# Kernel tuning notes

Measured on AMD Instinct MI355X. Metric: run time of the kernel, lower is better.

## Reference

```python
import jax, jax.numpy as jnp
import numpy as np

DIM = 1024
HEADS = 16
SCALE = DIM ** (-0.5)  # note: full dim, matching original module


def setup_inputs() -> dict:
    key = jax.random.key(0)
    k1, k2, k3, k4 = jax.random.split(key, 4)
    x = jax.random.normal(k1, (8, 1024, DIM), dtype=jnp.float32)
    w_qkv = jax.random.normal(k2, (DIM, 3 * DIM), dtype=jnp.float32) * (DIM ** -0.5)
    w_out = jax.random.normal(k3, (DIM, DIM), dtype=jnp.float32) * (DIM ** -0.5)
    b_out = jax.random.normal(k4, (DIM,), dtype=jnp.float32) * 0.01
    return {"x": x, "w_qkv": w_qkv, "w_out": w_out, "b_out": b_out}


def reference(x, w_qkv, w_out, b_out):
    b, n, dim = x.shape
    h = HEADS
    d = dim // h
    qkv = x @ w_qkv  # [b, n, 3*dim]
    q, k, v = jnp.split(qkv, 3, axis=-1)
    # 'b n (h d) -> b h n d'
    def to_heads(t):
        return t.reshape(b, n, h, d).transpose(0, 2, 1, 3)
    q, k, v = to_heads(q), to_heads(k), to_heads(v)
    dots = jnp.einsum('bhid,bhjd->bhij', q, k) * SCALE
    attn = jax.nn.softmax(dots, axis=-1)
    out = jnp.einsum('bhij,bhjd->bhid', attn, v)
    out = out.transpose(0, 2, 1, 3).reshape(b, n, dim)  # 'b h n d -> b n (h d)'
    return out @ w_out + b_out  # dropout is identity (rate=0 / eval)
```

## Files before the change

kernel.cpp:

```cpp
#include <hip/hip_runtime.h>

typedef __bf16 bf16x8 __attribute__((ext_vector_type(8)));
typedef __bf16 bf16x4 __attribute__((ext_vector_type(4)));
typedef float  f32x4  __attribute__((ext_vector_type(4)));

#define MFMA16(a, b, c) __builtin_amdgcn_mfma_f32_16x16x32_bf16(a, b, c, 0, 0, 0)
#define GLL(gp, lp) __builtin_amdgcn_global_load_lds( \
    (__attribute__((address_space(1))) void*)(gp),    \
    (__attribute__((address_space(3))) void*)(lp), 16, 0, 0)
#define WAITBAR(N) asm volatile("s_waitcnt vmcnt(" #N ") lgkmcnt(0)\n\ts_barrier" ::: "memory")

__global__ __launch_bounds__(256) void cast_x_kernel(const float* __restrict__ in,
                                                     __bf16* __restrict__ out) {
  int i = blockIdx.x * 256 + threadIdx.x;
  const float4 v = ((const float4*)in)[i];
  bf16x4 o = {(__bf16)v.x, (__bf16)v.y, (__bf16)v.z, (__bf16)v.w};
  ((bf16x4*)out)[i] = o;
}

__global__ void transpose_cast_kernel(const float* __restrict__ in,
                                      __bf16* __restrict__ out,
                                      int rows, int cols) {
  __shared__ float tile[32][33];
  int tx = threadIdx.x, ty = threadIdx.y;
  int x = blockIdx.x * 32 + tx;
  int y0 = blockIdx.y * 32;
#pragma unroll
  for (int i = 0; i < 32; i += 8)
    tile[ty + i][tx] = in[(y0 + ty + i) * cols + x];
  __syncthreads();
  int ox = y0 + tx;
  int oy0 = blockIdx.x * 32;
#pragma unroll
  for (int i = 0; i < 32; i += 8)
    out[(oy0 + ty + i) * rows + ox] = (__bf16)tile[tx][ty + i];
}

#define QSCALE 0.045084220027780106f
__global__ __launch_bounds__(256) void gemm_bt_kernel(
    const __bf16* __restrict__ A, const __bf16* __restrict__ Bt, int mode, int nxg,
    __bf16* __restrict__ qo, __bf16* __restrict__ ko, __bf16* __restrict__ vo,
    float* __restrict__ outp, const float* __restrict__ bias) {
  __shared__ __bf16 LDS[3][2][4096];
  const int tid = threadIdx.x;
  const int id = blockIdx.x;
  const int xcd = id & 7, s = id >> 3;
  const int bx = xcd * nxg + (nxg == 3 ? s % 3 : 0);
  const int by = (nxg == 3 ? s / 3 : s);
  const int m0 = by * 128, n0 = bx * 128;
  const int w = tid >> 6, lane = tid & 63;
  const int quad = lane >> 4, l15 = lane & 15;
  const int wm = (w >> 1) * 64, wn = (w & 1) * 64;
  f32x4 acc[4][4] = {};
  const int sr = tid >> 2;
  const int sc = (tid & 3) * 8;
  const __bf16* ag = A + (m0 + sr) * 1024 + sc;
  const __bf16* bg = Bt + (n0 + sr) * 1024 + sc;

  auto stage = [&](int T, int b) {
    const int kk = T * 32;
    GLL(ag + kk,             &LDS[b][0][0] + w * 512);
    GLL(ag + 64 * 1024 + kk, &LDS[b][0][0] + 2048 + w * 512);
    GLL(bg + kk,             &LDS[b][1][0] + w * 512);
    GLL(bg + 64 * 1024 + kk, &LDS[b][1][0] + 2048 + w * 512);
  };
  auto compute = [&](int b) {
    const __bf16* Asb = &LDS[b][0][0];
    const __bf16* Bsb = &LDS[b][1][0];
    bf16x8 af[4], bfr[4];
#pragma unroll
    for (int i = 0; i < 4; ++i)
      af[i] = *(const bf16x8*)(Asb + (wm + i * 16 + l15) * 32 + quad * 8);
#pragma unroll
    for (int j = 0; j < 4; ++j)
      bfr[j] = *(const bf16x8*)(Bsb + (wn + j * 16 + l15) * 32 + quad * 8);
#pragma unroll
    for (int i = 0; i < 4; ++i)
#pragma unroll
      for (int j = 0; j < 4; ++j)
        acc[i][j] = MFMA16(af[i], bfr[j], acc[i][j]);
  };

  stage(0, 0);
  stage(1, 1);
  WAITBAR(4);
  for (int g = 0; g < 10; ++g) {
    const int t = g * 3;
    stage(t + 2, 2); compute(0); WAITBAR(4);
    stage(t + 3, 0); compute(1); WAITBAR(4);
    stage(t + 4, 1); compute(2); WAITBAR(4);
  }
  compute(0);
  asm volatile("s_waitcnt vmcnt(0) lgkmcnt(0)\n\ts_barrier" ::: "memory");
  compute(1);
  __syncthreads();

  const int gcw = n0 + wn;
  float* T = (float*)(&LDS[0][0][0]) + w * 1088;
  if (mode == 0) {
    const int which = gcw >> 10;
    const int h = (gcw & 1023) >> 6;
    if (which == 2) {
#pragma unroll
      for (int i = 0; i < 4; ++i) {
        int gm = m0 + wm + i * 16 + quad * 4;
        int b = gm >> 10, n = gm & 1023;
        __bf16* vb = vo + ((long)(b * 16 + h) * 64) * 1024 + n;
#pragma unroll
        for (int j = 0; j < 4; ++j) {
          int dd = j * 16 + l15;
          bf16x4 pv = {(__bf16)acc[i][j][0], (__bf16)acc[i][j][1],
                       (__bf16)acc[i][j][2], (__bf16)acc[i][j][3]};
          *(bf16x4*)(vb + (long)dd * 1024) = pv;
        }
      }
    } else {
      __bf16* dst = (which == 0) ? qo : ko;
      const float scl = (which == 0) ? QSCALE : 1.0f;
#pragma unroll
      for (int i = 0; i < 4; ++i) {
#pragma unroll
        for (int j = 0; j < 4; ++j)
#pragma unroll
          for (int r = 0; r < 4; ++r)
            T[(quad * 4 + r) * 68 + j * 16 + l15] = acc[i][j][r];
        const float* Tr = T + l15 * 68 + quad * 16;
        f32x4 c0 = *(const f32x4*)(Tr);
        f32x4 c1 = *(const f32x4*)(Tr + 4);
        f32x4 c2 = *(const f32x4*)(Tr + 8);
        f32x4 c3 = *(const f32x4*)(Tr + 12);
        int gm = m0 + wm + i * 16 + l15;
        int b = gm >> 10, n = gm & 1023;
        __bf16* p = dst + ((long)((b * 16 + h) * 1024 + n)) * 64 + quad * 16;
        bf16x8 o0 = {(__bf16)(c0[0] * scl), (__bf16)(c0[1] * scl),
                     (__bf16)(c0[2] * scl), (__bf16)(c0[3] * scl),
                     (__bf16)(c1[0] * scl), (__bf16)(c1[1] * scl),
                     (__bf16)(c1[2] * scl), (__bf16)(c1[3] * scl)};
        bf16x8 o1 = {(__bf16)(c2[0] * scl), (__bf16)(c2[1] * scl),
                     (__bf16)(c2[2] * scl), (__bf16)(c2[3] * scl),
                     (__bf16)(c3[0] * scl), (__bf16)(c3[1] * scl),
                     (__bf16)(c3[2] * scl), (__bf16)(c3[3] * scl)};
        *(bf16x8*)p = o0;
        *(bf16x8*)(p + 8) = o1;
      }
    }
  } else {
    const int cb = gcw;
    f32x4 bv[4];
#pragma unroll
    for (int c = 0; c < 4; ++c)
      bv[c] = *(const f32x4*)(bias + cb + quad * 16 + c * 4);
#pragma unroll
    for (int i = 0; i < 4; ++i) {
#pragma unroll
      for (int j = 0; j < 4; ++j)
#pragma unroll
        for (int r = 0; r < 4; ++r)
          T[(quad * 4 + r) * 68 + j * 16 + l15] = acc[i][j][r];
      const float* Tr = T + l15 * 68 + quad * 16;
      int gm = m0 + wm + i * 16 + l15;
      float* p = outp + (long)gm * 1024 + cb + quad * 16;
#pragma unroll
      for (int c = 0; c < 4; ++c) {
        f32x4 v = *(const f32x4*)(Tr + c * 4);
        v += bv[c];
        *(f32x4*)(p + c * 4) = v;
      }
    }
  }
}

__global__ __launch_bounds__(256, 4) void attn_kernel(
    const __bf16* __restrict__ q, const __bf16* __restrict__ k,
    const __bf16* __restrict__ vt, __bf16* __restrict__ ao) {
  __shared__ __bf16 Ks[128 * 64];
  __shared__ __bf16 Vs[64 * 128];
  __shared__ __bf16 Ps[4][32 * 32];
  const int tid = threadIdx.x;
  const int bh = blockIdx.x & 127, qt = blockIdx.x >> 7;
  const int w = tid >> 6, lane = tid & 63;
  const int quad = lane >> 4, l15 = lane & 15;
  const int qrow = qt * 128 + w * 32;
  const __bf16* qb = q + (bh * 1024 + qrow) * 64;
  bf16x8 qf[2][2];
#pragma unroll
  for (int f = 0; f < 2; ++f) {
    qf[f][0] = *(const bf16x8*)(qb + (f * 16 + l15) * 64 + quad * 8);
    qf[f][1] = *(const bf16x8*)(qb + (f * 16 + l15) * 64 + 32 + quad * 8);
  }
  f32x4 o[2][4] = {};
  float rs0 = 0.f, rs1 = 0.f;
  const int krow = tid >> 3, kg8 = tid & 7;
  const __bf16* kg = k + (bh * 1024 + krow) * 64 + kg8 * 8;
  const int ksw = ((kg8 ^ (krow & 7)) * 8);
  const int vrow = tid >> 2, vg4 = tid & 3;
  const __bf16* vg = vt + (bh * 64 + vrow) * 1024 + vg4 * 8;
  const int kfs0 = (quad ^ (l15 & 7)) * 8;
  const int kfs1 = ((4 + quad) ^ (l15 & 7)) * 8;
  __bf16* pw = Ps[w];
  const int psw = quad ^ (l15 & 3);
  for (int j0 = 0; j0 < 1024; j0 += 128) {
    bf16x8 kv[4], vv[4];
#pragma unroll
    for (int p = 0; p < 4; ++p) kv[p] = *(const bf16x8*)(kg + (j0 + p * 32) * 64);
#pragma unroll
    for (int p = 0; p < 4; ++p) vv[p] = *(const bf16x8*)(vg + j0 + p * 32);
    __syncthreads();
#pragma unroll
    for (int p = 0; p < 4; ++p)
      *(bf16x8*)(Ks + (krow + p * 32) * 64 + ksw) = kv[p];
#pragma unroll
    for (int p = 0; p < 4; ++p)
      *(bf16x8*)(Vs + vrow * 128 + (((p * 4 + vg4) ^ (vrow & 15)) * 8)) = vv[p];
    __syncthreads();
    bf16x4 pk[2][8];
#pragma unroll
    for (int t = 0; t < 8; ++t) {
      const __bf16* kr = Ks + (t * 16 + l15) * 64;
      bf16x8 kf0 = *(const bf16x8*)(kr + kfs0);
      bf16x8 kf1 = *(const bf16x8*)(kr + kfs1);
      f32x4 z0 = {}, z1 = {};
      z0 = MFMA16(kf0, qf[0][0], z0);
      z0 = MFMA16(kf1, qf[0][1], z0);
      z1 = MFMA16(kf0, qf[1][0], z1);
      z1 = MFMA16(kf1, qf[1][1], z1);
      float p00 = exp2f(z0[0]), p01 = exp2f(z0[1]), p02 = exp2f(z0[2]), p03 = exp2f(z0[3]);
      float p10 = exp2f(z1[0]), p11 = exp2f(z1[1]), p12 = exp2f(z1[2]), p13 = exp2f(z1[3]);
      rs0 += (p00 + p01) + (p02 + p03);
      rs1 += (p10 + p11) + (p12 + p13);
      pk[0][t] = (bf16x4){(__bf16)p00, (__bf16)p01, (__bf16)p02, (__bf16)p03};
      pk[1][t] = (bf16x4){(__bf16)p10, (__bf16)p11, (__bf16)p12, (__bf16)p13};
    }
#pragma unroll
    for (int Q = 0; Q < 4; ++Q) {
#pragma unroll
      for (int f = 0; f < 2; ++f)
#pragma unroll
        for (int tl = 0; tl < 2; ++tl) {
          int g = (2 * tl + (quad >> 1)) ^ (l15 & 3);
          *(bf16x4*)(pw + (f * 16 + l15) * 32 + g * 8 + (quad & 1) * 4) = pk[f][2 * Q + tl];
        }
      bf16x8 pf0 = *(const bf16x8*)(pw + l15 * 32 + psw * 8);
      bf16x8 pf1 = *(const bf16x8*)(pw + (16 + l15) * 32 + psw * 8);
#pragma unroll
      for (int dt = 0; dt < 4; ++dt) {
        bf16x8 vf = *(const bf16x8*)(Vs + (dt * 16 + l15) * 128 + (((Q * 4 + quad) ^ l15) * 8));
        o[0][dt] = MFMA16(pf0, vf, o[0][dt]);
        o[1][dt] = MFMA16(pf1, vf, o[1][dt]);
      }
    }
  }
  rs0 += __shfl_xor(rs0, 16); rs0 += __shfl_xor(rs0, 32);
  rs1 += __shfl_xor(rs1, 16); rs1 += __shfl_xor(rs1, 32);
  const int b = bh >> 4, h = bh & 15;
  const int qbase = quad << 4;
#pragma unroll
  for (int r = 0; r < 4; ++r) {
    int src = qbase | (quad * 4 + r);
    float inv0 = 1.0f / __shfl(rs0, src);
    float inv1 = 1.0f / __shfl(rs1, src);
    long row0 = b * 1024 + qrow + quad * 4 + r;
    long row1 = row0 + 16;
#pragma unroll
    for (int dt = 0; dt < 4; ++dt) {
      ao[row0 * 1024 + h * 64 + dt * 16 + l15] = (__bf16)(o[0][dt][r] * inv0);
      ao[row1 * 1024 + h * 64 + dt * 16 + l15] = (__bf16)(o[1][dt][r] * inv1);
    }
  }
}

extern "C" void kernel_launch(void* const* d_in, const int* in_sizes, int n_in,
                              void* d_out, int out_size, void* d_ws, size_t ws_size,
                              hipStream_t stream) {
  const float* x = (const float*)d_in[0];
  const float* w_qkv = (const float*)d_in[1];
  const float* w_out = (const float*)d_in[2];
  const float* b_out = (const float*)d_in[3];
  float* out = (float*)d_out;

  char* ws = (char*)d_ws;
  __bf16* xb    = (__bf16*)(ws);
  __bf16* wqkvt = (__bf16*)(ws + 16777216);
  __bf16* woutt = (__bf16*)(ws + 23068672);
  __bf16* qw    = (__bf16*)(ws + 25165824);
  __bf16* kw    = (__bf16*)(ws + 41943040);
  __bf16* vw    = (__bf16*)(ws + 58720256);
  __bf16* ao    = xb;

  cast_x_kernel<<<8192, 256, 0, stream>>>(x, xb);
  transpose_cast_kernel<<<dim3(96, 32), dim3(32, 8), 0, stream>>>(w_qkv, wqkvt, 1024, 3072);
  transpose_cast_kernel<<<dim3(32, 32), dim3(32, 8), 0, stream>>>(w_out, woutt, 1024, 1024);
  gemm_bt_kernel<<<1536, 256, 0, stream>>>(xb, wqkvt, 0, 3, qw, kw, vw, nullptr, nullptr);
  attn_kernel<<<1024, 256, 0, stream>>>(qw, kw, vw, ao);
  gemm_bt_kernel<<<512, 256, 0, stream>>>(ao, woutt, 1, 1, nullptr, nullptr, nullptr, out, b_out);
}
```

Before: 277.3 us.

## Prefetch next K/V tile, interleave QK and PV, vectorize attention output stores

The attention kernel now issues global loads for the next K/V tile right after the LDS barrier, so they overlap with the current tile's compute instead of stalling at the top of each iteration. QK^T/exp generation is interleaved per Q-chunk with the PV MFMAs, with s_setprio raised around MFMA groups and the hardware exp2 builtin used. The output epilogue stages the accumulators through LDS to emit 16-byte bf16 stores instead of scattered 2-byte stores. This costs extra registers held across the loop and an added barrier plus LDS round trip at the end.

Measured after the change: 242.9 us. -12.4%, faster.

```diff
diff --git a/kernel.cpp b/kernel.cpp
--- a/kernel.cpp
+++ b/kernel.cpp
@@ -173,9 +173,10 @@
 __global__ __launch_bounds__(256, 4) void attn_kernel(
     const __bf16* __restrict__ q, const __bf16* __restrict__ k,
     const __bf16* __restrict__ vt, __bf16* __restrict__ ao) {
-  __shared__ __bf16 Ks[128 * 64];
-  __shared__ __bf16 Vs[64 * 128];
+  __shared__ __bf16 KV[2][128 * 64];
   __shared__ __bf16 Ps[4][32 * 32];
+  __bf16* const Ks = KV[0];
+  __bf16* const Vs = KV[1];
   const int tid = threadIdx.x;
   const int bh = blockIdx.x & 127, qt = blockIdx.x >> 7;
   const int w = tid >> 6, lane = tid & 63;
@@ -192,79 +193,102 @@
   float rs0 = 0.f, rs1 = 0.f;
   const int krow = tid >> 3, kg8 = tid & 7;
   const __bf16* kg = k + (bh * 1024 + krow) * 64 + kg8 * 8;
-  const int ksw = ((kg8 ^ (krow & 7)) * 8);
+  const int ksw = (kg8 ^ (krow & 7)) * 8;
   const int vrow = tid >> 2, vg4 = tid & 3;
   const __bf16* vg = vt + (bh * 64 + vrow) * 1024 + vg4 * 8;
   const int kfs0 = (quad ^ (l15 & 7)) * 8;
   const int kfs1 = ((4 + quad) ^ (l15 & 7)) * 8;
-  __bf16* pw = Ps[w];
+  __bf16* const pw = Ps[w];
   const int psw = quad ^ (l15 & 3);
-  for (int j0 = 0; j0 < 1024; j0 += 128) {
-    bf16x8 kv[4], vv[4];
-#pragma unroll
-    for (int p = 0; p < 4; ++p) kv[p] = *(const bf16x8*)(kg + (j0 + p * 32) * 64);
-#pragma unroll
-    for (int p = 0; p < 4; ++p) vv[p] = *(const bf16x8*)(vg + j0 + p * 32);
+
+  bf16x8 kvr[4], vvr[4];
+#pragma unroll
+  for (int p = 0; p < 4; ++p) kvr[p] = *(const bf16x8*)(kg + (p * 32) * 64);
+#pragma unroll
+  for (int p = 0; p < 4; ++p) vvr[p] = *(const bf16x8*)(vg + p * 32);
+
+  for (int jt = 0; jt < 8; ++jt) {
     __syncthreads();
 #pragma unroll
     for (int p = 0; p < 4; ++p)
-      *(bf16x8*)(Ks + (krow + p * 32) * 64 + ksw) = kv[p];
+      *(bf16x8*)(Ks + (krow + p * 32) * 64 + ksw) = kvr[p];
 #pragma unroll
     for (int p = 0; p < 4; ++p)
-      *(bf16x8*)(Vs + vrow * 128 + (((p * 4 + vg4) ^ (vrow & 15)) * 8)) = vv[p];
+      *(bf16x8*)(Vs + vrow * 128 + (((p * 4 + vg4) ^ (vrow & 15)) * 8)) = vvr[p];
     __syncthreads();
-    bf16x4 pk[2][8];
-#pragma unroll
-    for (int t = 0; t < 8; ++t) {
-      const __bf16* kr = Ks + (t * 16 + l15) * 64;
-      bf16x8 kf0 = *(const bf16x8*)(kr + kfs0);
-      bf16x8 kf1 = *(const bf16x8*)(kr + kfs1);
-      f32x4 z0 = {}, z1 = {};
-      z0 = MFMA16(kf0, qf[0][0], z0);
-      z0 = MFMA16(kf1, qf[0][1], z0);
-      z1 = MFMA16(kf0, qf[1][0], z1);
-      z1 = MFMA16(kf1, qf[1][1], z1);
-      float p00 = exp2f(z0[0]), p01 = exp2f(z0[1]), p02 = exp2f(z0[2]), p03 = exp2f(z0[3]);
-      float p10 = exp2f(z1[0]), p11 = exp2f(z1[1]), p12 = exp2f(z1[2]), p13 = exp2f(z1[3]);
-      rs0 += (p00 + p01) + (p02 + p03);
-      rs1 += (p10 + p11) + (p12 + p13);
-      pk[0][t] = (bf16x4){(__bf16)p00, (__bf16)p01, (__bf16)p02, (__bf16)p03};
-      pk[1][t] = (bf16x4){(__bf16)p10, (__bf16)p11, (__bf16)p12, (__bf16)p13};
+    if (jt < 7) {
+      const int j0n = (jt + 1) * 128;
+#pragma unroll
+      for (int p = 0; p < 4; ++p) kvr[p] = *(const bf16x8*)(kg + (j0n + p * 32) * 64);
+#pragma unroll
+      for (int p = 0; p < 4; ++p) vvr[p] = *(const bf16x8*)(vg + j0n + p * 32);
     }
 #pragma unroll
     for (int Q = 0; Q < 4; ++Q) {
 #pragma unroll
-      for (int f = 0; f < 2; ++f)
-#pragma unroll
-        for (int tl = 0; tl < 2; ++tl) {
-          int g = (2 * tl + (quad >> 1)) ^ (l15 & 3);
-          *(bf16x4*)(pw + (f * 16 + l15) * 32 + g * 8 + (quad & 1) * 4) = pk[f][2 * Q + tl];
-        }
+      for (int tl = 0; tl < 2; ++tl) {
+        const int t = 2 * Q + tl;
+        const __bf16* kr = Ks + (t * 16 + l15) * 64;
+        bf16x8 kf0 = *(const bf16x8*)(kr + kfs0);
+        bf16x8 kf1 = *(const bf16x8*)(kr + kfs1);
+        f32x4 z0 = {}, z1 = {};
+        __builtin_amdgcn_s_setprio(1);
+        z0 = MFMA16(kf0, qf[0][0], z0);
+        z0 = MFMA16(kf1, qf[0][1], z0);
+        z1 = MFMA16(kf0, qf[1][0], z1);
+        z1 = MFMA16(kf1, qf[1][1], z1);
+        __builtin_amdgcn_s_setprio(0);
+        const float p00 = __builtin_amdgcn_exp2f(z0[0]), p01 = __builtin_amdgcn_exp2f(z0[1]);
+        const float p02 = __builtin_amdgcn_exp2f(z0[2]), p03 = __builtin_amdgcn_exp2f(z0[3]);
+        const float p10 = __builtin_amdgcn_exp2f(z1[0]), p11 = __builtin_amdgcn_exp2f(z1[1]);
+        const float p12 = __builtin_amdgcn_exp2f(z1[2]), p13 = __builtin_amdgcn_exp2f(z1[3]);
+        rs0 += (p00 + p01) + (p02 + p03);
+        rs1 += (p10 + p11) + (p12 + p13);
+        const int g = (2 * tl + (quad >> 1)) ^ (l15 & 3);
+        bf16x4 pa = {(__bf16)p00, (__bf16)p01, (__bf16)p02, (__bf16)p03};
+        bf16x4 pb = {(__bf16)p10, (__bf16)p11, (__bf16)p12, (__bf16)p13};
+        *(bf16x4*)(pw + l15 * 32 + g * 8 + (quad & 1) * 4) = pa;
+        *(bf16x4*)(pw + (16 + l15) * 32 + g * 8 + (quad & 1) * 4) = pb;
+      }
       bf16x8 pf0 = *(const bf16x8*)(pw + l15 * 32 + psw * 8);
       bf16x8 pf1 = *(const bf16x8*)(pw + (16 + l15) * 32 + psw * 8);
+      __builtin_amdgcn_s_setprio(1);
 #pragma unroll
       for (int dt = 0; dt < 4; ++dt) {
         bf16x8 vf = *(const bf16x8*)(Vs + (dt * 16 + l15) * 128 + (((Q * 4 + quad) ^ l15) * 8));
         o[0][dt] = MFMA16(pf0, vf, o[0][dt]);
         o[1][dt] = MFMA16(pf1, vf, o[1][dt]);
       }
+      __builtin_amdgcn_s_setprio(0);
     }
   }
   rs0 += __shfl_xor(rs0, 16); rs0 += __shfl_xor(rs0, 32);
   rs1 += __shfl_xor(rs1, 16); rs1 += __shfl_xor(rs1, 32);
+  __syncthreads();
+  float* const T = (float*)KV + w * 1088;
   const int b = bh >> 4, h = bh & 15;
-  const int qbase = quad << 4;
-#pragma unroll
-  for (int r = 0; r < 4; ++r) {
-    int src = qbase | (quad * 4 + r);
-    float inv0 = 1.0f / __shfl(rs0, src);
-    float inv1 = 1.0f / __shfl(rs1, src);
-    long row0 = b * 1024 + qrow + quad * 4 + r;
-    long row1 = row0 + 16;
-#pragma unroll
-    for (int dt = 0; dt < 4; ++dt) {
-      ao[row0 * 1024 + h * 64 + dt * 16 + l15] = (__bf16)(o[0][dt][r] * inv0);
-      ao[row1 * 1024 + h * 64 + dt * 16 + l15] = (__bf16)(o[1][dt][r] * inv1);
+  const int rr = lane >> 3, c8 = lane & 7;
+#pragma unroll
+  for (int f = 0; f < 2; ++f) {
+    const float rsf = f ? rs1 : rs0;
+#pragma unroll
+    for (int dt = 0; dt < 4; ++dt)
+#pragma unroll
+      for (int r = 0; r < 4; ++r)
+        T[(quad * 4 + r) * 68 + dt * 16 + l15] = o[f][dt][r];
+#pragma unroll
+    for (int h2 = 0; h2 < 2; ++h2) {
+      const int row = h2 * 8 + rr;
+      const float inv = 1.0f / __shfl(rsf, row);
+      const float* Tr = T + row * 68 + c8 * 8;
+      const f32x4 a0 = *(const f32x4*)(Tr);
+      const f32x4 a1 = *(const f32x4*)(Tr + 4);
+      bf16x8 ov = {(__bf16)(a0[0] * inv), (__bf16)(a0[1] * inv),
+                   (__bf16)(a0[2] * inv), (__bf16)(a0[3] * inv),
+                   (__bf16)(a1[0] * inv), (__bf16)(a1[1] * inv),
+                   (__bf16)(a1[2] * inv), (__bf16)(a1[3] * inv)};
+      const long grow = (long)b * 1024 + qrow + f * 16 + row;
+      *(bf16x8*)(ao + grow * 1024 + h * 64 + c8 * 8) = ov;
     }
   }
 }
```
